# Optimization experiments

Measured on AMD Instinct MI355X. Metric: run time of the kernel, lower is better.

Reference implementation:

```python
import jax, jax.numpy as jnp
import numpy as np

A = 1.0
B = 1.0
DT = 0.01
INTENSITY = 1.0


def setup_inputs() -> dict:
    key = jax.random.key(0)
    k1, k2 = jax.random.split(key)
    x = jax.random.normal(k1, (64, 64, 4096), dtype=jnp.float32)
    noise = jax.random.normal(k2, (64, 64, 4096), dtype=jnp.float32)
    return {"x": x, "noise": noise}


def reference(x, noise):
    # x, noise: (batch, channels, time_steps)
    dt = jnp.float32(DT)
    sqrt_dt = jnp.sqrt(dt)
    a = jnp.float32(A)
    b = jnp.float32(B)
    intensity = jnp.float32(INTENSITY)

    def f(y, i_val):
        return a * y - b * y ** 3 + i_val

    def step(state, xn):
        inp, n = xn
        k1 = f(state, inp)
        k2 = f(state + 0.5 * dt * k1, inp)
        k3 = f(state + 0.5 * dt * k2, inp)
        k4 = f(state + dt * k3, inp)
        new_state = state + dt / 6.0 * (k1 + 2.0 * k2 + 2.0 * k3 + k4) + intensity * n * sqrt_dt
        return new_state, new_state

    # scan over time axis: move time to leading dim -> (T, B, C)
    xt = jnp.moveaxis(x, -1, 0)
    nt = jnp.moveaxis(noise, -1, 0)
    state0 = jnp.zeros(x.shape[:2], dtype=x.dtype)
    _, outs = jax.lax.scan(step, state0, (xt, nt))
    return jnp.moveaxis(outs, 0, -1)  # (B, C, T)
```

## Files before the change

kernel.cpp:

```cpp
#include <hip/hip_runtime.h>


#define T_STEPS 4096
#define TILE    64
#define NTILES  (T_STEPS / TILE)
#define N_SEQ   4096

typedef float f32x4 __attribute__((ext_vector_type(4)));

__device__ __forceinline__ float rk4_step(float s, float i, float n) {
    const float H  = 0.01f;
    const float H2 = 0.005f;
    const float H6 = 0.01f / 6.0f;
    const float SD = 0.1f;

    float c1    = fmaf(H2, i, s);
    float c3    = fmaf(H,  i, s);
    float basei = fmaf(H6, i, fmaf(SD, n, s));

    float u1 = s * s;
    float p1 = H2 * s;
    float w1 = 1.0f - u1;
    float k1 = fmaf(s, w1, i);
    float y2 = fmaf(p1, w1, c1);

    float u2 = y2 * y2;
    float p2 = H2 * y2;
    float w2 = 1.0f - u2;
    float k2 = fmaf(y2, w2, i);
    float y3 = fmaf(p2, w2, c1);

    float u3 = y3 * y3;
    float p3 = H * y3;
    float w3 = 1.0f - u3;
    float k3 = fmaf(y3, w3, i);
    float y4 = fmaf(p3, w3, c3);

    float t12   = fmaf(2.0f, k2, k1);
    float tsum  = fmaf(2.0f, k3, t12);
    float base2 = fmaf(H6, tsum, basei);

    float u4 = y4 * y4;
    float z4 = H6 * y4;
    float w4 = 1.0f - u4;
    return fmaf(z4, w4, base2);
}

__global__ __launch_bounds__(64, 1) void bistable_sr_kernel(
        const float* __restrict__ x,
        const float* __restrict__ noise,
        float* __restrict__ out) {
    __shared__ f32x4 lx[TILE * 16];
    __shared__ f32x4 ln[TILE * 16];

    const int l  = threadIdx.x;
    const int rl = l >> 4;
    const int sl = l & 15;
    const int xorl = l & 7;
    const size_t sb = (size_t)blockIdx.x * 64;

    f32x4 xr[16], nr[16];
#pragma unroll
    for (int m = 0; m < 16; ++m) {
        const size_t g = (sb + 4 * m + rl) * T_STEPS + sl * 4;
        xr[m] = *(const f32x4*)(x + g);
        nr[m] = *(const f32x4*)(noise + g);
    }

    float s = 0.0f;
    float* po = out + (sb + l) * T_STEPS;

    for (int tau = 0; tau < NTILES; ++tau) {
#pragma unroll
        for (int m = 0; m < 16; ++m) {
            const int row  = 4 * m + rl;
            const int slot = sl ^ (row & 7);
            lx[row * 16 + slot] = xr[m];
            ln[row * 16 + slot] = nr[m];
        }

        const int nt = (tau + 1 < NTILES) ? tau + 1 : tau;
#pragma unroll
        for (int m = 0; m < 16; ++m) {
            const size_t g = (sb + 4 * m + rl) * T_STEPS
                           + (size_t)nt * TILE + sl * 4;
            xr[m] = *(const f32x4*)(x + g);
            nr[m] = *(const f32x4*)(noise + g);
        }

#pragma unroll
        for (int j = 0; j < 16; ++j) {
            const int idx = l * 16 + (j ^ xorl);
            f32x4 xv = lx[idx];
            f32x4 nv = ln[idx];
            f32x4 o;
            s = rk4_step(s, xv.x, nv.x); o.x = s;
            s = rk4_step(s, xv.y, nv.y); o.y = s;
            s = rk4_step(s, xv.z, nv.z); o.z = s;
            s = rk4_step(s, xv.w, nv.w); o.w = s;
            *(f32x4*)(po + tau * TILE + j * 4) = o;
        }
    }
}

extern "C" void kernel_launch(void* const* d_in, const int* in_sizes, int n_in,
                              void* d_out, int out_size, void* d_ws, size_t ws_size,
                              hipStream_t stream) {
    const float* x     = (const float*)d_in[0];
    const float* noise = (const float*)d_in[1];
    float* out = (float*)d_out;

    dim3 grid(N_SEQ / 64);
    dim3 block(64);
    bistable_sr_kernel<<<grid, block, 0, stream>>>(x, noise, out);
}
```

Before: 234.6 us.

## Split compute and memory into producer/consumer wavefronts with double-buffered LDS

Each block now runs two wavefronts. One does only the serial RK4 recurrence reading from LDS, and the other prefetches input tiles into double-buffered LDS and writes finished output tiles from an LDS staging buffer back to global memory with coalesced stores. The tile shrinks to 32 time steps so the two buffers fit. This aims to take global load/store latency and uncoalesced per-thread output stores off the serial compute path. In exchange it adds a block-wide barrier every tile and puts more LDS traffic on the critical path.

```diff
diff --git a/kernel.cpp b/kernel.cpp
--- a/kernel.cpp
+++ b/kernel.cpp
@@ -2,9 +2,11 @@
 
 
 #define T_STEPS 4096
-#define TILE    64
-#define NTILES  (T_STEPS / TILE)
 #define N_SEQ   4096
+#define TILE    32
+#define NT      (T_STEPS / TILE)
+#define ROW_BYTES (T_STEPS * 4)
+#define TB      (TILE * 4)
 
 typedef float f32x4 __attribute__((ext_vector_type(4)));
 
@@ -46,59 +48,108 @@
     return fmaf(z4, w4, base2);
 }
 
-__global__ __launch_bounds__(64, 1) void bistable_sr_kernel(
+__global__ __launch_bounds__(128, 1) void bistable_sr_kernel(
         const float* __restrict__ x,
         const float* __restrict__ noise,
         float* __restrict__ out) {
-    __shared__ f32x4 lx[TILE * 16];
-    __shared__ f32x4 ln[TILE * 16];
+    __shared__ f32x4 ibx[2][512];
+    __shared__ f32x4 ibn[2][512];
+    __shared__ f32x4 obf[2][512];
 
-    const int l  = threadIdx.x;
-    const int rl = l >> 4;
-    const int sl = l & 15;
-    const int xorl = l & 7;
+    const int tid = threadIdx.x;
+    const int wid = tid >> 6;
+    const int l   = tid & 63;
     const size_t sb = (size_t)blockIdx.x * 64;
 
-    f32x4 xr[16], nr[16];
+    const char* xb = (const char*)(x + sb * T_STEPS);
+    const char* nb = (const char*)(noise + sb * T_STEPS);
+    char*       ob = (char*)(out + sb * T_STEPS);
+
+    int goff[8];
 #pragma unroll
-    for (int m = 0; m < 16; ++m) {
-        const size_t g = (sb + 4 * m + rl) * T_STEPS + sl * 4;
-        xr[m] = *(const f32x4*)(x + g);
-        nr[m] = *(const f32x4*)(noise + g);
+    for (int k = 0; k < 8; ++k) {
+        const int r = 8 * k + (l >> 3);
+        goff[k] = r * ROW_BYTES + (((l & 7) ^ (r & 7)) << 4);
     }
 
+    f32x4 xr[8], nr[8];
+    if (wid == 1) {
+#pragma unroll
+        for (int k = 0; k < 8; ++k) {
+            xr[k] = *(const f32x4*)(xb + goff[k]);
+            nr[k] = *(const f32x4*)(nb + goff[k]);
+        }
+#pragma unroll
+        for (int k = 0; k < 8; ++k) {
+            ibx[0][k * 64 + l] = xr[k];
+            ibn[0][k * 64 + l] = nr[k];
+        }
+#pragma unroll
+        for (int k = 0; k < 8; ++k) {
+            xr[k] = *(const f32x4*)(xb + goff[k] + TB);
+            nr[k] = *(const f32x4*)(nb + goff[k] + TB);
+        }
+    }
+
+    const int xorl = l & 7;
     float s = 0.0f;
-    float* po = out + (sb + l) * T_STEPS;
 
-    for (int tau = 0; tau < NTILES; ++tau) {
+    __syncthreads();
+
+    for (int tau = 0; tau < NT; ++tau) {
+        const int b = tau & 1;
+        if (wid == 0) {
+            const f32x4* px = &ibx[b][l * 8];
+            const f32x4* pn = &ibn[b][l * 8];
+            f32x4*       po = &obf[b][l * 8];
+
+            f32x4 xv = px[0 ^ xorl], nv = pn[0 ^ xorl];
 #pragma unroll
-        for (int m = 0; m < 16; ++m) {
-            const int row  = 4 * m + rl;
-            const int slot = sl ^ (row & 7);
-            lx[row * 16 + slot] = xr[m];
-            ln[row * 16 + slot] = nr[m];
+            for (int j = 0; j < 8; ++j) {
+                f32x4 xv2, nv2;
+                if (j < 7) {
+                    xv2 = px[(j + 1) ^ xorl];
+                    nv2 = pn[(j + 1) ^ xorl];
+                }
+                f32x4 o;
+                s = rk4_step(s, xv.x, nv.x); o.x = s;
+                s = rk4_step(s, xv.y, nv.y); o.y = s;
+                s = rk4_step(s, xv.z, nv.z); o.z = s;
+                s = rk4_step(s, xv.w, nv.w); o.w = s;
+                po[j ^ xorl] = o;
+                xv = xv2; nv = nv2;
+            }
+        } else {
+            if (tau + 1 < NT) {
+#pragma unroll
+                for (int k = 0; k < 8; ++k) {
+                    ibx[b ^ 1][k * 64 + l] = xr[k];
+                    ibn[b ^ 1][k * 64 + l] = nr[k];
+                }
+                if (tau + 2 < NT) {
+#pragma unroll
+                    for (int k = 0; k < 8; ++k) {
+                        xr[k] = *(const f32x4*)(xb + goff[k] + (tau + 2) * TB);
+                        nr[k] = *(const f32x4*)(nb + goff[k] + (tau + 2) * TB);
+                    }
+                }
+            }
+            if (tau >= 1) {
+#pragma unroll
+                for (int k = 0; k < 8; ++k) {
+                    f32x4 v = obf[(tau - 1) & 1][k * 64 + l];
+                    *(f32x4*)(ob + goff[k] + (tau - 1) * TB) = v;
+                }
+            }
         }
+        __syncthreads();
+    }
 
-        const int nt = (tau + 1 < NTILES) ? tau + 1 : tau;
+    if (wid == 1) {
 #pragma unroll
-        for (int m = 0; m < 16; ++m) {
-            const size_t g = (sb + 4 * m + rl) * T_STEPS
-                           + (size_t)nt * TILE + sl * 4;
-            xr[m] = *(const f32x4*)(x + g);
-            nr[m] = *(const f32x4*)(noise + g);
-        }
-
-#pragma unroll
-        for (int j = 0; j < 16; ++j) {
-            const int idx = l * 16 + (j ^ xorl);
-            f32x4 xv = lx[idx];
-            f32x4 nv = ln[idx];
-            f32x4 o;
-            s = rk4_step(s, xv.x, nv.x); o.x = s;
-            s = rk4_step(s, xv.y, nv.y); o.y = s;
-            s = rk4_step(s, xv.z, nv.z); o.z = s;
-            s = rk4_step(s, xv.w, nv.w); o.w = s;
-            *(f32x4*)(po + tau * TILE + j * 4) = o;
+        for (int k = 0; k < 8; ++k) {
+            f32x4 v = obf[(NT - 1) & 1][k * 64 + l];
+            *(f32x4*)(ob + goff[k] + (NT - 1) * TB) = v;
         }
     }
 }
@@ -111,6 +162,6 @@
     float* out = (float*)d_out;
 
     dim3 grid(N_SEQ / 64);
-    dim3 block(64);
+    dim3 block(128);
     bistable_sr_kernel<<<grid, block, 0, stream>>>(x, noise, out);
 }
```

Measured after the change: 201.6 us. 1.16x faster.
